# Performance work log

Measured on AMD Instinct MI355X. Metric: run time of the kernel, lower is better.

The kernel has to match this reference:

```python
import jax, jax.numpy as jnp
import numpy as np

N_HEADS = 8  # from init_kwargs; only used for the softmax scale


def setup_inputs() -> dict:
    key = jax.random.key(0)
    k1, k2, k3 = jax.random.split(key, 3)
    B, S, D = 4, 4096, 1024
    inputs = jax.random.normal(k1, (B, S, 2 * D), dtype=jnp.float32)
    W_qkv = jax.random.normal(k2, (2 * D, 3 * D), dtype=jnp.float32) * (1.0 / np.sqrt(2 * D))
    W_ff = jax.random.normal(k3, (D, D), dtype=jnp.float32) * (1.0 / np.sqrt(D))
    b_ff = jnp.zeros((D,), dtype=jnp.float32)
    return {"inputs": inputs, "W_qkv": W_qkv, "W_ff": W_ff, "b_ff": b_ff}


def reference(inputs, W_qkv, W_ff, b_ff):
    D = W_ff.shape[0]
    dim_head = D / N_HEADS
    scale = 1.0 / np.sqrt(dim_head)
    kqv = inputs @ W_qkv                       # [B, S, 3D]
    k, q, v = jnp.split(kqv, 3, axis=-1)        # chunk order in source: k, q, v
    scores = jnp.einsum('bqd,bkd->bqk', q, k) * scale   # [B, S, S]
    attn = jax.nn.softmax(scores, axis=-1)
    # dropout_p is undefined in the buggy source; treated as eval-mode identity
    out = jnp.einsum('bqk,bkd->bqd', attn, v)   # [B, S, D]
    return out @ W_ff + b_ff
```

## Files before the change

kernel.cpp:

```cpp
#include <hip/hip_runtime.h>

typedef unsigned short u16;
using bf16x8 = __attribute__((ext_vector_type(8))) __bf16;
using f32x4  = __attribute__((ext_vector_type(4))) float;
using u16x8  = __attribute__((ext_vector_type(8))) u16;

__device__ __forceinline__ u16 f2bf(float f) {
    unsigned u = __builtin_bit_cast(unsigned, f);
    u += 0x7FFFu + ((u >> 16) & 1u);
    return (u16)(u >> 16);
}
__device__ __forceinline__ float bf2f(u16 h) {
    unsigned u = ((unsigned)h) << 16;
    return __builtin_bit_cast(float, u);
}
__device__ __forceinline__ u16 to_bf(float f) { return f2bf(f); }
__device__ __forceinline__ u16 to_bf(u16 h)   { return h; }

__device__ __forceinline__ void gload_lds16(const u16* g, u16* l) {
    __builtin_amdgcn_global_load_lds(
        (const __attribute__((address_space(1))) unsigned int*)g,
        (__attribute__((address_space(3))) unsigned int*)l,
        16, 0, 0);
}

__global__ __launch_bounds__(256) void k_cvt_f32_bf16(const float* __restrict__ in,
                                                      u16* __restrict__ out, long n) {
    long i = ((long)blockIdx.x * 256 + threadIdx.x) * 8;
    if (i + 8 > n) return;
    f32x4 a = *(const f32x4*)(in + i);
    f32x4 b = *(const f32x4*)(in + i + 4);
    u16x8 o;
    o[0] = f2bf(a[0]); o[1] = f2bf(a[1]); o[2] = f2bf(a[2]); o[3] = f2bf(a[3]);
    o[4] = f2bf(b[0]); o[5] = f2bf(b[1]); o[6] = f2bf(b[2]); o[7] = f2bf(b[3]);
    *(u16x8*)(out + i) = o;
}

template <typename T>
__global__ __launch_bounds__(256) void k_transpose_bf16(
    const T* __restrict__ in, long in_rs, long in_bs,
    u16* __restrict__ out, long out_rs, long out_bs, int R, int C) {
    __shared__ u16 tile[32][33];
    const int b = blockIdx.z;
    const T* ip = in + (long)b * in_bs;
    u16* op = out + (long)b * out_bs;
    const int tx = threadIdx.x, ty = threadIdx.y;
    const long r0 = (long)blockIdx.y * 32, c0 = (long)blockIdx.x * 32;
#pragma unroll
    for (int i = 0; i < 4; ++i) {
        int r = ty + i * 8;
        tile[r][tx] = to_bf(ip[(r0 + r) * in_rs + c0 + tx]);
    }
    __syncthreads();
#pragma unroll
    for (int i = 0; i < 4; ++i) {
        int c = ty + i * 8;
        op[(c0 + c) * out_rs + r0 + tx] = tile[tx][c];
    }
}

__global__ __launch_bounds__(256) void k_psum_recip(const float* __restrict__ psum,
                                                    float* __restrict__ rrow,
                                                    int nx, long total) {
    long idx = (long)blockIdx.x * 256 + threadIdx.x;
    if (idx >= total) return;
    const long z = idx >> 12, row = idx & 4095;
    const float* p = psum + (z * nx) * 4096 + row;
    float s = 0.f;
    for (int x = 0; x < nx; ++x) s += p[(long)x * 4096];
    rrow[idx] = 1.0f / s;
}


#define VMC(n) asm volatile("s_waitcnt vmcnt(" #n ")" ::: "memory")
#define SCHB   __builtin_amdgcn_sched_barrier(0)
#define BAR    __builtin_amdgcn_s_barrier()
#define PRIO1  __builtin_amdgcn_s_setprio(1)
#define PRIO0  __builtin_amdgcn_s_setprio(0)
#define SWZ(b) ((b) ^ ((((b) >> 9) & 1) << 5))

template <int EPI>
__global__ __launch_bounds__(512, 4) void k_gemm3b(
    const u16* __restrict__ Ag, long lda, long sA,
    const u16* __restrict__ Bg, long ldb, long sB,
    void* __restrict__ Cv, long ldc, long sC,
    int K, float scale, const float* __restrict__ rrowZ, long sR,
    const float* __restrict__ bias, float* __restrict__ psum, int nx) {
    __shared__ __align__(16) u16 As[3][128 * 32];
    __shared__ __align__(16) u16 Bs[3][256 * 32];

    const int tid = threadIdx.x;
    const int lane = tid & 63, wid = tid >> 6;
    const int wm = wid >> 2, wn = wid & 3;
    const int z = blockIdx.z;
    const int nwg = gridDim.x;
    const int bid = blockIdx.x;
    const int swzb = (bid & 7) * (nwg >> 3) + (bid >> 3);
    const int bx = swzb % nx, by = swzb / nx;
    const long m0 = (long)by * 128;
    const long n0 = (long)bx * 256;
    const u16* A = Ag + (long)z * sA;
    const u16* B = Bg + (long)z * sB;

    long aSrc, bSrc0, bSrc1;
    {
        int dg = SWZ(tid * 16);
        aSrc = (m0 + (dg >> 6)) * lda + ((dg & 63) >> 1);
        bSrc0 = (n0 + (dg >> 6)) * ldb + ((dg & 63) >> 1);
        dg = SWZ(8192 + tid * 16);
        bSrc1 = (n0 + (dg >> 6)) * ldb + ((dg & 63) >> 1);
    }
    const int r16 = lane & 15, g = lane >> 4;
    const int vA = SWZ((wm * 64 + r16) * 64 + g * 16);
    const int vB = SWZ((wn * 64 + r16) * 64 + g * 16);

#define STG(bb, kt) do { \
        gload_lds16(A + aSrc + (kt), &As[bb][wid * 512]); \
        gload_lds16(B + bSrc0 + (kt), &Bs[bb][wid * 512]); \
        gload_lds16(B + bSrc1 + (kt), &Bs[bb][4096 + wid * 512]); } while (0)
#define LD4_A(bb) do { _Pragma("unroll") for (int _i = 0; _i < 4; ++_i) \
        afr[_i] = *(const bf16x8*)((const char*)&As[bb][0] + vA + _i * 1024); } while (0)
#define LD4_B(bb) do { _Pragma("unroll") for (int _i = 0; _i < 4; ++_i) \
        bfr[_i] = *(const bf16x8*)((const char*)&Bs[bb][0] + vB + _i * 1024); } while (0)
#define MM16() do { \
        _Pragma("unroll") for (int mf = 0; mf < 4; ++mf) \
        _Pragma("unroll") for (int nf = 0; nf < 4; ++nf) \
            acc[mf][nf] = __builtin_amdgcn_mfma_f32_16x16x32_bf16( \
                afr[mf], bfr[nf], acc[mf][nf], 0, 0, 0); } while (0)

    f32x4 acc[4][4] = {};
    bf16x8 afr[4], bfr[4];

    const int NT = K >> 5;
    STG(0, 0); STG(1, 32);
    VMC(3); SCHB;
    BAR; SCHB;

    int b0 = 0, b1 = 1, b2 = 2;
    for (int t = 0; t < NT; ++t) {
        LD4_A(b0); LD4_B(b0);
        if (t + 2 < NT) STG(b2, (long)(t + 2) * 32);
        PRIO1; MM16(); PRIO0;
        if (t + 2 < NT) { VMC(3); }
        else if (t + 1 < NT) { VMC(0); }
        BAR; SCHB;
        int tm = b0; b0 = b1; b1 = b2; b2 = tm;
    }

    const int r_in = (lane >> 4) * 4;
    const int c_in = lane & 15;
    const float* rr = (EPI == 2) ? (rrowZ + (long)z * sR) : nullptr;
    float rsum[4][4];
    if constexpr (EPI == 1) {
#pragma unroll
        for (int a = 0; a < 4; ++a)
#pragma unroll
            for (int b = 0; b < 4; ++b) rsum[a][b] = 0.f;
    }
#pragma unroll
    for (int mf = 0; mf < 4; ++mf) {
#pragma unroll
        for (int nf = 0; nf < 4; ++nf) {
            const long cg = n0 + wn * 64 + nf * 16 + c_in;
#pragma unroll
            for (int j = 0; j < 4; ++j) {
                const long rg = m0 + wm * 64 + mf * 16 + r_in + j;
                float v = acc[mf][nf][j];
                if constexpr (EPI == 0) {
                    ((u16*)Cv)[(long)z * sC + rg * ldc + cg] = f2bf(v);
                } else if constexpr (EPI == 1) {
                    float e = __expf(v * scale);
                    ((u16*)Cv)[(long)z * sC + rg * ldc + cg] = f2bf(e);
                    rsum[mf][j] += e;
                } else if constexpr (EPI == 2) {
                    ((u16*)Cv)[(long)z * sC + rg * ldc + cg] = f2bf(v * rr[rg]);
                } else {
                    ((float*)Cv)[(long)z * sC + rg * ldc + cg] = v + bias[cg];
                }
            }
        }
    }
    if constexpr (EPI == 1) {
        float* ps = (float*)&As[0][0];
#pragma unroll
        for (int mf = 0; mf < 4; ++mf) {
#pragma unroll
            for (int j = 0; j < 4; ++j) {
                float s = rsum[mf][j];
#pragma unroll
                for (int w = 1; w < 16; w <<= 1) s += __shfl_xor(s, w);
                if ((lane & 15) == 0)
                    ps[(wm * 64 + mf * 16 + (lane >> 4) * 4 + j) * 4 + wn] = s;
            }
        }
        __syncthreads();
        if (tid < 128) {
            float s = ps[tid * 4] + ps[tid * 4 + 1] + ps[tid * 4 + 2] + ps[tid * 4 + 3];
            const long M = (long)(nwg / nx) * 128;
            psum[((long)z * nx + bx) * M + m0 + tid] = s;
        }
    }
#undef MM16
#undef LD4_A
#undef LD4_B
#undef STG
}

extern "C" void kernel_launch(void* const* d_in, const int* in_sizes, int n_in,
                              void* d_out, int out_size, void* d_ws, size_t ws_size,
                              hipStream_t stream) {
    (void)in_sizes; (void)n_in; (void)out_size;
    const int S = 4096;
    const long BS = 4L * S;
    const float* x_f    = (const float*)d_in[0];
    const float* Wqkv_f = (const float*)d_in[1];
    const float* Wff_f  = (const float*)d_in[2];
    const float* bff    = (const float*)d_in[3];
    float* out = (float*)d_out;

    const size_t need4 = 67108864UL + 12582912UL + 2097152UL + 100663296UL +
                         33554432UL + 4UL * 33554432UL + 33554432UL + 65536UL +
                         4UL * 16 * 4096 * 4;
    const bool batched = ws_size >= need4;
    const int Z = batched ? 4 : 1;

    char* p = (char*)d_ws;
    u16* x_bf  = (u16*)p; p += BS * 2048 * 2;
    u16* WqkvT = (u16*)p; p += 3072L * 2048 * 2;
    u16* WffT  = (u16*)p; p += 1024L * 1024 * 2;
    u16* kqv   = (u16*)p; p += BS * 3072 * 2;
    u16* vT    = (u16*)p; p += 4L * 1024 * 4096 * 2;
    u16* probs = (u16*)p; p += (long)Z * 4096L * 4096 * 2;
    u16* attn  = (u16*)p; p += BS * 1024 * 2;
    float* rrow = (float*)p; p += (long)Z * 4096L * 4;
    float* psum = (float*)p; p += (long)Z * 16 * 4096 * 4;

    k_cvt_f32_bf16<<<dim3((unsigned)(BS * 2048 / 2048)), 256, 0, stream>>>(x_f, x_bf, BS * 2048);
    k_transpose_bf16<float><<<dim3(3072 / 32, 2048 / 32, 1), dim3(32, 8), 0, stream>>>(
        Wqkv_f, 3072, 0, WqkvT, 2048, 0, 2048, 3072);
    k_transpose_bf16<float><<<dim3(1024 / 32, 1024 / 32, 1), dim3(32, 8), 0, stream>>>(
        Wff_f, 1024, 0, WffT, 1024, 0, 1024, 1024);

    k_gemm3b<0><<<dim3(12 * 128, 1, 1), 512, 0, stream>>>(
        x_bf, 2048, 0, WqkvT, 2048, 0, kqv, 3072, 0, 2048, 0.f, nullptr, 0,
        nullptr, nullptr, 12);

    k_transpose_bf16<u16><<<dim3(1024 / 32, 4096 / 32, 4), dim3(32, 8), 0, stream>>>(
        kqv + 2048, 3072, (long)S * 3072, vT, 4096, 1024L * 4096, 4096, 1024);

    const float scale = 0.08838834764831845f;
    for (int b = 0; b < 4; b += Z) {
        const u16* kbase = kqv + (long)b * S * 3072;
        k_gemm3b<1><<<dim3(16 * 32, 1, Z), 512, 0, stream>>>(
            kbase + 1024, 3072, (long)S * 3072, kbase, 3072, (long)S * 3072,
            probs, 4096, (long)S * S, 1024, scale, nullptr, 0, nullptr, psum, 16);
        k_psum_recip<<<(Z * 4096 + 255) / 256, 256, 0, stream>>>(
            psum, rrow, 16, (long)Z * 4096);
        k_gemm3b<2><<<dim3(4 * 32, 1, Z), 512, 0, stream>>>(
            probs, 4096, (long)S * S, vT + (long)b * 1024 * 4096, 4096, 1024L * 4096,
            attn + (long)b * S * 1024, 1024, (long)S * 1024,
            4096, 0.f, rrow, 4096, nullptr, nullptr, 4);
    }

    k_gemm3b<3><<<dim3(4 * 128, 1, 1), 512, 0, stream>>>(
        attn, 1024, 0, WffT, 1024, 0, out, 1024, 0, 1024, 0.f, nullptr, 0,
        bff, nullptr, 4);
}
```

Before: 606.2 us.

## Fuse fp32-to-bf16 input conversion into the QKV GEMM A-tile load

```diff
diff --git a/kernel.cpp b/kernel.cpp
--- a/kernel.cpp
+++ b/kernel.cpp
@@ -22,18 +22,6 @@
         (const __attribute__((address_space(1))) unsigned int*)g,
         (__attribute__((address_space(3))) unsigned int*)l,
         16, 0, 0);
-}
-
-__global__ __launch_bounds__(256) void k_cvt_f32_bf16(const float* __restrict__ in,
-                                                      u16* __restrict__ out, long n) {
-    long i = ((long)blockIdx.x * 256 + threadIdx.x) * 8;
-    if (i + 8 > n) return;
-    f32x4 a = *(const f32x4*)(in + i);
-    f32x4 b = *(const f32x4*)(in + i + 4);
-    u16x8 o;
-    o[0] = f2bf(a[0]); o[1] = f2bf(a[1]); o[2] = f2bf(a[2]); o[3] = f2bf(a[3]);
-    o[4] = f2bf(b[0]); o[5] = f2bf(b[1]); o[6] = f2bf(b[2]); o[7] = f2bf(b[3]);
-    *(u16x8*)(out + i) = o;
 }
 
 template <typename T>
@@ -73,15 +61,16 @@
 
 
 #define VMC(n) asm volatile("s_waitcnt vmcnt(" #n ")" ::: "memory")
+#define LGK0   asm volatile("s_waitcnt lgkmcnt(0)" ::: "memory")
 #define SCHB   __builtin_amdgcn_sched_barrier(0)
 #define BAR    __builtin_amdgcn_s_barrier()
 #define PRIO1  __builtin_amdgcn_s_setprio(1)
 #define PRIO0  __builtin_amdgcn_s_setprio(0)
 #define SWZ(b) ((b) ^ ((((b) >> 9) & 1) << 5))
 
-template <int EPI>
+template <int EPI, bool CVTA>
 __global__ __launch_bounds__(512, 4) void k_gemm3b(
-    const u16* __restrict__ Ag, long lda, long sA,
+    const void* __restrict__ Av, long lda, long sA,
     const u16* __restrict__ Bg, long ldb, long sB,
     void* __restrict__ Cv, long ldc, long sC,
     int K, float scale, const float* __restrict__ rrowZ, long sR,
@@ -99,25 +88,44 @@
     const int bx = swzb % nx, by = swzb / nx;
     const long m0 = (long)by * 128;
     const long n0 = (long)bx * 256;
-    const u16* A = Ag + (long)z * sA;
+    const u16* A16 = (const u16*)Av + (long)z * sA;
+    const float* A32 = (const float*)Av + (long)z * sA;
     const u16* B = Bg + (long)z * sB;
 
-    long aSrc, bSrc0, bSrc1;
+    long aSrc = 0, bSrc0, bSrc1;
+    long aOffF = 0; int wA = 0;
     {
         int dg = SWZ(tid * 16);
-        aSrc = (m0 + (dg >> 6)) * lda + ((dg & 63) >> 1);
+        if constexpr (!CVTA) aSrc = (m0 + (dg >> 6)) * lda + ((dg & 63) >> 1);
         bSrc0 = (n0 + (dg >> 6)) * ldb + ((dg & 63) >> 1);
         dg = SWZ(8192 + tid * 16);
         bSrc1 = (n0 + (dg >> 6)) * ldb + ((dg & 63) >> 1);
     }
+    if constexpr (CVTA) {
+        const int rowA = tid >> 2, kbA = (tid & 3) * 8;
+        aOffF = (m0 + rowA) * lda + kbA;
+        wA = SWZ(rowA * 64 + kbA * 2);
+    }
     const int r16 = lane & 15, g = lane >> 4;
     const int vA = SWZ((wm * 64 + r16) * 64 + g * 16);
     const int vB = SWZ((wn * 64 + r16) * 64 + g * 16);
 
-#define STG(bb, kt) do { \
-        gload_lds16(A + aSrc + (kt), &As[bb][wid * 512]); \
+#define STG3(bb, kt) do { \
+        gload_lds16(A16 + aSrc + (kt), &As[bb][wid * 512]); \
         gload_lds16(B + bSrc0 + (kt), &Bs[bb][wid * 512]); \
         gload_lds16(B + bSrc1 + (kt), &Bs[bb][4096 + wid * 512]); } while (0)
+#define STGB(bb, kt) do { \
+        gload_lds16(B + bSrc0 + (kt), &Bs[bb][wid * 512]); \
+        gload_lds16(B + bSrc1 + (kt), &Bs[bb][4096 + wid * 512]); } while (0)
+#define ALD(L0, L1, kt) do { \
+        L0 = *(const f32x4*)(A32 + aOffF + (kt)); \
+        L1 = *(const f32x4*)(A32 + aOffF + (kt) + 4); } while (0)
+#define ACVW(U0, U1, bb) do { u16x8 _o; \
+        _o[0] = f2bf(U0[0]); _o[1] = f2bf(U0[1]); \
+        _o[2] = f2bf(U0[2]); _o[3] = f2bf(U0[3]); \
+        _o[4] = f2bf(U1[0]); _o[5] = f2bf(U1[1]); \
+        _o[6] = f2bf(U1[2]); _o[7] = f2bf(U1[3]); \
+        *(u16x8*)((char*)&As[bb][0] + wA) = _o; } while (0)
 #define LD4_A(bb) do { _Pragma("unroll") for (int _i = 0; _i < 4; ++_i) \
         afr[_i] = *(const bf16x8*)((const char*)&As[bb][0] + vA + _i * 1024); } while (0)
 #define LD4_B(bb) do { _Pragma("unroll") for (int _i = 0; _i < 4; ++_i) \
@@ -132,19 +140,49 @@
     bf16x8 afr[4], bfr[4];
 
     const int NT = K >> 5;
-    STG(0, 0); STG(1, 32);
-    VMC(3); SCHB;
-    BAR; SCHB;
-
     int b0 = 0, b1 = 1, b2 = 2;
-    for (int t = 0; t < NT; ++t) {
-        LD4_A(b0); LD4_B(b0);
-        if (t + 2 < NT) STG(b2, (long)(t + 2) * 32);
-        PRIO1; MM16(); PRIO0;
-        if (t + 2 < NT) { VMC(3); }
-        else if (t + 1 < NT) { VMC(0); }
+
+    if constexpr (CVTA) {
+        f32x4 rA00, rA01, rA10, rA11;
+        STGB(0, 0); ALD(rA00, rA01, 0);
+        STGB(1, 32); ALD(rA10, rA11, 32);
+        VMC(4); SCHB;
+        ACVW(rA00, rA01, 0);
+        VMC(0); SCHB;
+        ACVW(rA10, rA11, 1);
+        LGK0;
         BAR; SCHB;
-        int tm = b0; b0 = b1; b1 = b2; b2 = tm;
+
+#define ASUB(tt, L0, L1, U0, U1) do { \
+        LD4_A(b0); LD4_B(b0); \
+        if ((tt) + 2 < NT) { STGB(b2, (long)((tt) + 2) * 32); \
+                             ALD(L0, L1, (long)((tt) + 2) * 32); } \
+        PRIO1; MM16(); PRIO0; \
+        if ((tt) + 2 < NT) { VMC(4); } \
+        else if ((tt) + 1 < NT) { VMC(0); } \
+        SCHB; \
+        if ((tt) >= 1 && (tt) + 1 < NT) { ACVW(U0, U1, b1); LGK0; } \
+        BAR; SCHB; \
+        { int _tm = b0; b0 = b1; b1 = b2; b2 = _tm; } } while (0)
+
+        for (int t = 0; t < NT; t += 2) {
+            ASUB(t, rA00, rA01, rA10, rA11);
+            ASUB(t + 1, rA10, rA11, rA00, rA01);
+        }
+#undef ASUB
+    } else {
+        STG3(0, 0); STG3(1, 32);
+        VMC(3); SCHB;
+        BAR; SCHB;
+        for (int t = 0; t < NT; ++t) {
+            LD4_A(b0); LD4_B(b0);
+            if (t + 2 < NT) STG3(b2, (long)(t + 2) * 32);
+            PRIO1; MM16(); PRIO0;
+            if (t + 2 < NT) { VMC(3); }
+            else if (t + 1 < NT) { VMC(0); }
+            BAR; SCHB;
+            int tm = b0; b0 = b1; b1 = b2; b2 = tm;
+        }
     }
 
     const int r_in = (lane >> 4) * 4;
@@ -203,7 +241,10 @@
 #undef MM16
 #undef LD4_A
 #undef LD4_B
-#undef STG
+#undef ACVW
+#undef ALD
+#undef STGB
+#undef STG3
 }
 
 extern "C" void kernel_launch(void* const* d_in, const int* in_sizes, int n_in,
@@ -218,14 +259,13 @@
     const float* bff    = (const float*)d_in[3];
     float* out = (float*)d_out;
 
-    const size_t need4 = 67108864UL + 12582912UL + 2097152UL + 100663296UL +
+    const size_t need4 = 12582912UL + 2097152UL + 100663296UL +
                          33554432UL + 4UL * 33554432UL + 33554432UL + 65536UL +
                          4UL * 16 * 4096 * 4;
     const bool batched = ws_size >= need4;
     const int Z = batched ? 4 : 1;
 
     char* p = (char*)d_ws;
-    u16* x_bf  = (u16*)p; p += BS * 2048 * 2;
     u16* WqkvT = (u16*)p; p += 3072L * 2048 * 2;
     u16* WffT  = (u16*)p; p += 1024L * 1024 * 2;
     u16* kqv   = (u16*)p; p += BS * 3072 * 2;
@@ -235,14 +275,13 @@
     float* rrow = (float*)p; p += (long)Z * 4096L * 4;
     float* psum = (float*)p; p += (long)Z * 16 * 4096 * 4;
 
-    k_cvt_f32_bf16<<<dim3((unsigned)(BS * 2048 / 2048)), 256, 0, stream>>>(x_f, x_bf, BS * 2048);
     k_transpose_bf16<float><<<dim3(3072 / 32, 2048 / 32, 1), dim3(32, 8), 0, stream>>>(
         Wqkv_f, 3072, 0, WqkvT, 2048, 0, 2048, 3072);
     k_transpose_bf16<float><<<dim3(1024 / 32, 1024 / 32, 1), dim3(32, 8), 0, stream>>>(
         Wff_f, 1024, 0, WffT, 1024, 0, 1024, 1024);
 
-    k_gemm3b<0><<<dim3(12 * 128, 1, 1), 512, 0, stream>>>(
-        x_bf, 2048, 0, WqkvT, 2048, 0, kqv, 3072, 0, 2048, 0.f, nullptr, 0,
+    k_gemm3b<0, true><<<dim3(12 * 128, 1, 1), 512, 0, stream>>>(
+        x_f, 2048, 0, WqkvT, 2048, 0, kqv, 3072, 0, 2048, 0.f, nullptr, 0,
         nullptr, nullptr, 12);
 
     k_transpose_bf16<u16><<<dim3(1024 / 32, 4096 / 32, 4), dim3(32, 8), 0, stream>>>(
@@ -251,18 +290,18 @@
     const float scale = 0.08838834764831845f;
     for (int b = 0; b < 4; b += Z) {
         const u16* kbase = kqv + (long)b * S * 3072;
-        k_gemm3b<1><<<dim3(16 * 32, 1, Z), 512, 0, stream>>>(
+        k_gemm3b<1, false><<<dim3(16 * 32, 1, Z), 512, 0, stream>>>(
             kbase + 1024, 3072, (long)S * 3072, kbase, 3072, (long)S * 3072,
             probs, 4096, (long)S * S, 1024, scale, nullptr, 0, nullptr, psum, 16);
         k_psum_recip<<<(Z * 4096 + 255) / 256, 256, 0, stream>>>(
             psum, rrow, 16, (long)Z * 4096);
-        k_gemm3b<2><<<dim3(4 * 32, 1, Z), 512, 0, stream>>>(
+        k_gemm3b<2, false><<<dim3(4 * 32, 1, Z), 512, 0, stream>>>(
             probs, 4096, (long)S * S, vT + (long)b * 1024 * 4096, 4096, 1024L * 4096,
             attn + (long)b * S * 1024, 1024, (long)S * 1024,
             4096, 0.f, rrow, 4096, nullptr, nullptr, 4);
     }
 
-    k_gemm3b<3><<<dim3(4 * 128, 1, 1), 512, 0, stream>>>(
+    k_gemm3b<3, false><<<dim3(4 * 128, 1, 1), 512, 0, stream>>>(
         attn, 1024, 0, WffT, 1024, 0, out, 1024, 0, 1024, 0.f, nullptr, 0,
         bff, nullptr, 4);
 }
```

Result: slower. 695.7 us (+14.8%).
